# Optimization experiments

Measured on AMD Instinct MI355X. Metric: run time of the kernel, lower is better.

The kernel has to match this reference:

```python
import jax, jax.numpy as jnp
import numpy as np

HIDDEN = 64
N_HEADS = 4
TOP_K = 10
ALPHA = 0.3


def setup_inputs() -> dict:
    key = jax.random.key(0)
    ks = jax.random.split(key, 12)
    B, N, T, Dd, Ds, H = 4, 2048, 32, 16, 8, HIDDEN
    s = lambda i, shape, scale: (jax.random.normal(ks[i], shape, dtype=jnp.float32) * scale)
    return {
        "x_dyn": jax.random.normal(ks[0], (B, N, T, Dd), dtype=jnp.float32),
        "x_stat": jax.random.normal(ks[1], (B, N, Ds), dtype=jnp.float32),
        "A_prior": jax.random.uniform(ks[2], (B, N, N), dtype=jnp.float32),
        "W_dyn": s(3, (Dd, H), 1.0 / np.sqrt(Dd)),
        "b_dyn": jnp.zeros((H,), jnp.float32),
        "W_stat": s(4, (Ds, H), 1.0 / np.sqrt(Ds)),
        "b_stat": jnp.zeros((H,), jnp.float32),
        "W_fuse": s(5, (2 * H, H), 1.0 / np.sqrt(2 * H)),
        "b_fuse": jnp.zeros((H,), jnp.float32),
        "Wq": s(6, (H, H), 1.0 / np.sqrt(H)),
        "Wk": s(7, (H, H), 1.0 / np.sqrt(H)),
    }


def reference(x_dyn, x_stat, A_prior, W_dyn, b_dyn, W_stat, b_stat, W_fuse, b_fuse, Wq, Wk):
    B, N = x_dyn.shape[0], x_dyn.shape[1]
    H, nh = HIDDEN, N_HEADS
    dh = H // nh

    # TemporalEncoder: linear + mean over time + ReLU -> (B, N, H)
    h = jax.nn.relu(jnp.mean(x_dyn @ W_dyn + b_dyn, axis=2))
    # FeatureEncoder: linear + ReLU -> (B, N, H)
    h_s = jax.nn.relu(x_stat @ W_stat + b_stat)
    # Fusion
    h = jnp.concatenate([h, h_s], axis=-1) @ W_fuse + b_fuse

    # GraphAttention: multi-head softmax(QK^T / sqrt(dh)) averaged over heads
    q = (h @ Wq).reshape(B, N, nh, dh)
    k = (h @ Wk).reshape(B, N, nh, dh)
    scores = jnp.einsum("bnhd,bmhd->bhnm", q, k) / jnp.sqrt(jnp.float32(dh))
    A_learn = jnp.mean(jax.nn.softmax(scores, axis=-1), axis=1)  # (B, N, N)

    # Top-k mask along last dim (scatter 1s at topk indices)
    _, topk_inds = jax.lax.top_k(A_learn, TOP_K)  # (B, N, k)
    b_idx = jnp.arange(B)[:, None, None]
    n_idx = jnp.arange(N)[None, :, None]
    mask = jnp.zeros_like(A_learn).at[b_idx, n_idx, topk_inds].set(1.0)
    A_sparse = A_learn * mask
    A_learn = (A_sparse + jnp.swapaxes(A_sparse, 1, 2)) * 0.5

    # Blend with prior
    A_final = ALPHA * A_prior + (1.0 - ALPHA) * A_learn

    # Laplacian L = D - A
    degree = jnp.sum(A_final, axis=-1)  # (B, N)
    eye = jnp.eye(N, dtype=A_final.dtype)
    L = degree[..., None] * eye - A_final
    return (L, A_final)
```

## Files before the change

kernel.cpp:

```cpp
#include <hip/hip_runtime.h>

#define NBATCH 4
#define NN 2048
#define NR 8192
#define TOPK 10
#define CSTRIDE 321

typedef __attribute__((ext_vector_type(16))) float f32x16;
typedef __attribute__((ext_vector_type(8))) short bf16x8;

__device__ inline unsigned short f2bf(float x) {
    unsigned u = __float_as_uint(x);
    unsigned r = (u + 0x7FFF + ((u >> 16) & 1)) >> 16;
    return (unsigned short)r;
}

__global__ __launch_bounds__(256) void k13(
    const float* __restrict__ xd, const float* __restrict__ xs,
    const float* __restrict__ Wd, const float* __restrict__ bd,
    const float* __restrict__ Ws, const float* __restrict__ bs,
    const float* __restrict__ Wf, const float* __restrict__ bf,
    const float* __restrict__ Wq, const float* __restrict__ Wk,
    unsigned short* __restrict__ qh, unsigned short* __restrict__ kh,
    const float* __restrict__ prior, float* __restrict__ Lout,
    float* __restrict__ Aout)
{
    if (blockIdx.x >= NR/4) {
        int r = blockIdx.x - NR/4;
        __shared__ float wsum[4];
        const float4* pr = (const float4*)(prior + (size_t)r * NN);
        float4* Ar = (float4*)(Aout + (size_t)r * NN);
        float4* Lr = (float4*)(Lout + (size_t)r * NN);
        float sum = 0.f;
        for (int i = threadIdx.x; i < NN/4; i += 256) {
            float4 p = pr[i];
            float4 a; a.x = 0.3f*p.x; a.y = 0.3f*p.y; a.z = 0.3f*p.z; a.w = 0.3f*p.w;
            Ar[i] = a;
            float4 lv; lv.x = -a.x; lv.y = -a.y; lv.z = -a.z; lv.w = -a.w;
            Lr[i] = lv;
            sum += a.x + a.y + a.z + a.w;
        }
        #pragma unroll
        for (int o = 32; o > 0; o >>= 1) sum += __shfl_down(sum, o);
        if ((threadIdx.x & 63) == 0) wsum[threadIdx.x >> 6] = sum;
        __syncthreads();
        if (threadIdx.x == 0) {
            float tot = wsum[0] + wsum[1] + wsum[2] + wsum[3];
            atomicAdd(&Lout[(size_t)r * NN + (r & 2047)], tot);
        }
        return;
    }

    int wave = threadIdx.x >> 6;
    int lane = threadIdx.x & 63;
    int r = blockIdx.x * 4 + wave;

    __shared__ float xm[4][16];
    __shared__ float xst[4][8];
    __shared__ float hc[4][128];
    __shared__ float hh[4][64];

    const float* xdr = xd + (size_t)r * 512;
    float acc = 0.f;
    #pragma unroll
    for (int j = 0; j < 8; ++j) acc += xdr[lane + 64*j];
    acc += __shfl_xor(acc, 16);
    acc += __shfl_xor(acc, 32);
    if (lane < 16) xm[wave][lane] = acc * (1.0f/32.0f);
    if (lane < 8)  xst[wave][lane] = xs[(size_t)r*8 + lane];
    __syncthreads();

    float a1 = bd[lane];
    #pragma unroll
    for (int d = 0; d < 16; ++d) a1 += xm[wave][d] * Wd[d*64 + lane];
    a1 = fmaxf(a1, 0.f);
    float a2 = bs[lane];
    #pragma unroll
    for (int d = 0; d < 8; ++d) a2 += xst[wave][d] * Ws[d*64 + lane];
    a2 = fmaxf(a2, 0.f);
    hc[wave][lane] = a1;
    hc[wave][64 + lane] = a2;
    __syncthreads();

    float hv0 = bf[lane], hv1 = 0.f, hv2 = 0.f, hv3 = 0.f;
    #pragma unroll
    for (int j = 0; j < 128; j += 4) {
        hv0 += hc[wave][j]   * Wf[(j)*64   + lane];
        hv1 += hc[wave][j+1] * Wf[(j+1)*64 + lane];
        hv2 += hc[wave][j+2] * Wf[(j+2)*64 + lane];
        hv3 += hc[wave][j+3] * Wf[(j+3)*64 + lane];
    }
    hh[wave][lane] = (hv0 + hv1) + (hv2 + hv3);
    __syncthreads();

    float qv0 = 0.f, qv1 = 0.f, kv0 = 0.f, kv1 = 0.f;
    #pragma unroll
    for (int j = 0; j < 64; j += 2) {
        float h0 = hh[wave][j], h1 = hh[wave][j+1];
        qv0 += h0 * Wq[(j)*64   + lane];
        qv1 += h1 * Wq[(j+1)*64 + lane];
        kv0 += h0 * Wk[(j)*64   + lane];
        kv1 += h1 * Wk[(j+1)*64 + lane];
    }
    float qv = qv0 + qv1, kv = kv0 + kv1;
    int b = r >> 11, n = r & 2047;
    int head = lane >> 4, dim = lane & 15;
    size_t base = ((size_t)(b*4 + head) * NN + n) * 16;
    qh[base + dim] = f2bf(qv);
    kh[base + dim] = f2bf(kv);
}

__global__ __launch_bounds__(1024, 4) void k2_fused(
    const unsigned short* __restrict__ qh, const unsigned short* __restrict__ kh,
    float* __restrict__ Lout, float* __restrict__ Aout)
{
    const float C1 = 0.36067376022224085f;
    int b  = blockIdx.x >> 6;
    int rg = blockIdx.x & 63;
    int tid = threadIdx.x;
    int w = tid >> 6, l = tid & 63;
    int row = l & 31, khalf = l >> 5;

    __shared__ unsigned cand[32 * CSTRIDE];
    __shared__ float redS[16][4][32];
    __shared__ float r4s[4][32];

    bf16x8 qfrag[4];
    #pragma unroll
    for (int h = 0; h < 4; ++h)
        qfrag[h] = *(const bf16x8*)(qh + ((size_t)(b*4+h) * NN + rg*32 + row) * 16 + khalf*8);

    float Sl[4] = {0.f, 0.f, 0.f, 0.f};
    for (int t = 0; t < 4; ++t) {
        int m0 = w*128 + t*32;
        #pragma unroll
        for (int h = 0; h < 4; ++h) {
            bf16x8 kfrag = *(const bf16x8*)(kh + ((size_t)(b*4+h) * NN + m0 + row) * 16 + khalf*8);
            f32x16 acc = {0.f,0.f,0.f,0.f,0.f,0.f,0.f,0.f,0.f,0.f,0.f,0.f,0.f,0.f,0.f,0.f};
            acc = __builtin_amdgcn_mfma_f32_32x32x16_bf16(kfrag, qfrag[h], acc, 0, 0, 0);
            #pragma unroll
            for (int rr = 0; rr < 16; ++rr) Sl[h] += exp2f(acc[rr] * C1);
        }
    }
    #pragma unroll
    for (int h = 0; h < 4; ++h) Sl[h] += __shfl_xor(Sl[h], 32);
    if (l < 32) {
        #pragma unroll
        for (int h = 0; h < 4; ++h) redS[w][h][l] = Sl[h];
    }
    __syncthreads();
    if (tid < 128) {
        int h = tid >> 5, rw = tid & 31;
        float s = 0.f;
        #pragma unroll
        for (int ww = 0; ww < 16; ++ww) s += redS[ww][h][rw];
        r4s[h][rw] = 0.25f / s;
    }
    __syncthreads();

    float r4[4];
    #pragma unroll
    for (int h = 0; h < 4; ++h) r4[h] = r4s[h][row];

    unsigned tkl[TOPK];
    #pragma unroll
    for (int s = 0; s < TOPK; ++s) tkl[s] = 0u;
    for (int t = 0; t < 4; ++t) {
        int m0 = w*128 + t*32;
        float vacc[16];
        #pragma unroll
        for (int rr = 0; rr < 16; ++rr) vacc[rr] = 0.f;
        #pragma unroll
        for (int h = 0; h < 4; ++h) {
            bf16x8 kfrag = *(const bf16x8*)(kh + ((size_t)(b*4+h) * NN + m0 + row) * 16 + khalf*8);
            f32x16 acc = {0.f,0.f,0.f,0.f,0.f,0.f,0.f,0.f,0.f,0.f,0.f,0.f,0.f,0.f,0.f,0.f};
            acc = __builtin_amdgcn_mfma_f32_32x32x16_bf16(kfrag, qfrag[h], acc, 0, 0, 0);
            #pragma unroll
            for (int rr = 0; rr < 16; ++rr)
                vacc[rr] = fmaf(exp2f(acc[rr] * C1), r4[h], vacc[rr]);
        }
        #pragma unroll
        for (int rr = 0; rr < 16; ++rr) {
            int c = m0 + ((rr & 3) + 8*(rr >> 2) + 4*khalf);
            unsigned key = ((unsigned)f2bf(vacc[rr]) << 16) | (unsigned)(2047 - c);
            if (key > tkl[TOPK-1]) {
                unsigned ck = key;
                #pragma unroll
                for (int s = 0; s < TOPK; ++s) {
                    bool ins = ck > tkl[s];
                    unsigned o = tkl[s];
                    tkl[s] = ins ? ck : o;
                    ck     = ins ? o  : ck;
                }
            }
        }
    }
    {
        unsigned* cr = &cand[row * CSTRIDE + (w*2 + khalf) * TOPK];
        #pragma unroll
        for (int s = 0; s < TOPK; ++s) cr[s] = tkl[s];
    }
    __syncthreads();

    #pragma unroll 1
    for (int rr2 = 0; rr2 < 2; ++rr2) {
        int prow = w*2 + rr2;
        const unsigned* flat = &cand[prow * CSTRIDE];
        unsigned tk5[5];
        #pragma unroll
        for (int i = 0; i < 5; ++i) tk5[i] = flat[l*5 + i];
        unsigned mykey = 0u;
        #pragma unroll 1
        for (int s = 0; s < TOPK; ++s) {
            unsigned kmax = tk5[0];
            #pragma unroll
            for (int d = 1; d < 64; d <<= 1) {
                unsigned o = __shfl_xor(kmax, d);
                kmax = (o > kmax) ? o : kmax;
            }
            if (tk5[0] == kmax) {
                #pragma unroll
                for (int q = 0; q < 4; ++q) tk5[q] = tk5[q+1];
                tk5[4] = 0u;
            }
            if (l == s) mykey = kmax;
        }

        int n = rg*32 + prow;
        size_t rbase = (size_t)(b*NN + n) * NN;
        float wv = 0.f;
        int j = 0;
        if (l < TOPK) {
            wv = 0.35f * __uint_as_float(mykey & 0xFFFF0000u);
            j = 2047 - (int)(mykey & 0x7FFu);
        }
        float swv = wv;
        #pragma unroll
        for (int d = 1; d <= 8; d <<= 1) swv += __shfl_xor(swv, d);
        if (l == 0) atomicAdd(&Lout[rbase + n], swv);
        if (l < TOPK) {
            size_t jbase = (size_t)(b*NN + j) * NN;
            atomicAdd(&Aout[rbase + j],  wv);
            atomicAdd(&Aout[jbase + n],  wv);
            atomicAdd(&Lout[rbase + j], -wv);
            atomicAdd(&Lout[jbase + n], -wv);
            atomicAdd(&Lout[jbase + j],  wv);
        }
    }
}

extern "C" void kernel_launch(void* const* d_in, const int* in_sizes, int n_in,
                              void* d_out, int out_size, void* d_ws, size_t ws_size,
                              hipStream_t stream)
{
    const float* xd    = (const float*)d_in[0];
    const float* xs    = (const float*)d_in[1];
    const float* prior = (const float*)d_in[2];
    const float* Wd    = (const float*)d_in[3];
    const float* bd    = (const float*)d_in[4];
    const float* Ws    = (const float*)d_in[5];
    const float* bs    = (const float*)d_in[6];
    const float* Wf    = (const float*)d_in[7];
    const float* bf    = (const float*)d_in[8];
    const float* Wq    = (const float*)d_in[9];
    const float* Wk    = (const float*)d_in[10];

    float* Lout = (float*)d_out;
    float* Aout = Lout + (size_t)NR * NN;

    unsigned short* qh = (unsigned short*)d_ws;
    unsigned short* kh = qh + (size_t)16 * NN * 16;

    k13<<<NR/4 + NR, 256, 0, stream>>>(xd, xs, Wd, bd, Ws, bs, Wf, bf, Wq, Wk,
                                       qh, kh, prior, Lout, Aout);
    k2_fused<<<NBATCH*64, 1024, 0, stream>>>(qh, kh, Lout, Aout);
}
```

Baseline: 324.0 us.

## Overlap prior blend with attention kernel and defer top-k scatter to separate kernel

Moves the prior-blend/Laplacian-init blocks from the encoder kernel into the attention/top-k kernel so the bandwidth-bound streaming overlaps with the MFMA-heavy score computation. The attention blocks shrink from 1024 to 512 threads, each wave covering twice the columns. Top-k winners are written to a workspace buffer and scattered by a new third kernel, which also avoids racing the atomics against the prior initialisation. This adds one launch and a small workspace round trip, and gives fewer waves per attention block.

```diff
diff --git a/kernel.cpp b/kernel.cpp
--- a/kernel.cpp
+++ b/kernel.cpp
@@ -4,7 +4,7 @@
 #define NN 2048
 #define NR 8192
 #define TOPK 10
-#define CSTRIDE 321
+#define CSTRIDE 161
 
 typedef __attribute__((ext_vector_type(16))) float f32x16;
 typedef __attribute__((ext_vector_type(8))) short bf16x8;
@@ -15,42 +15,14 @@
     return (unsigned short)r;
 }
 
-__global__ __launch_bounds__(256) void k13(
+__global__ __launch_bounds__(256) void k1_encode(
     const float* __restrict__ xd, const float* __restrict__ xs,
     const float* __restrict__ Wd, const float* __restrict__ bd,
     const float* __restrict__ Ws, const float* __restrict__ bs,
     const float* __restrict__ Wf, const float* __restrict__ bf,
     const float* __restrict__ Wq, const float* __restrict__ Wk,
-    unsigned short* __restrict__ qh, unsigned short* __restrict__ kh,
-    const float* __restrict__ prior, float* __restrict__ Lout,
-    float* __restrict__ Aout)
-{
-    if (blockIdx.x >= NR/4) {
-        int r = blockIdx.x - NR/4;
-        __shared__ float wsum[4];
-        const float4* pr = (const float4*)(prior + (size_t)r * NN);
-        float4* Ar = (float4*)(Aout + (size_t)r * NN);
-        float4* Lr = (float4*)(Lout + (size_t)r * NN);
-        float sum = 0.f;
-        for (int i = threadIdx.x; i < NN/4; i += 256) {
-            float4 p = pr[i];
-            float4 a; a.x = 0.3f*p.x; a.y = 0.3f*p.y; a.z = 0.3f*p.z; a.w = 0.3f*p.w;
-            Ar[i] = a;
-            float4 lv; lv.x = -a.x; lv.y = -a.y; lv.z = -a.z; lv.w = -a.w;
-            Lr[i] = lv;
-            sum += a.x + a.y + a.z + a.w;
-        }
-        #pragma unroll
-        for (int o = 32; o > 0; o >>= 1) sum += __shfl_down(sum, o);
-        if ((threadIdx.x & 63) == 0) wsum[threadIdx.x >> 6] = sum;
-        __syncthreads();
-        if (threadIdx.x == 0) {
-            float tot = wsum[0] + wsum[1] + wsum[2] + wsum[3];
-            atomicAdd(&Lout[(size_t)r * NN + (r & 2047)], tot);
-        }
-        return;
-    }
-
+    unsigned short* __restrict__ qh, unsigned short* __restrict__ kh)
+{
     int wave = threadIdx.x >> 6;
     int lane = threadIdx.x & 63;
     int r = blockIdx.x * 4 + wave;
@@ -110,19 +82,47 @@
     kh[base + dim] = f2bf(kv);
 }
 
-__global__ __launch_bounds__(1024, 4) void k2_fused(
+__global__ __launch_bounds__(512, 4) void k23(
     const unsigned short* __restrict__ qh, const unsigned short* __restrict__ kh,
-    float* __restrict__ Lout, float* __restrict__ Aout)
+    unsigned* __restrict__ winners, float* __restrict__ diagw,
+    const float* __restrict__ prior, float* __restrict__ Lout,
+    float* __restrict__ Aout)
 {
     const float C1 = 0.36067376022224085f;
+    int tid = threadIdx.x;
+
+    if (blockIdx.x >= 256) {
+        int r = blockIdx.x - 256;
+        __shared__ float wsum[8];
+        const float4* pr = (const float4*)(prior + (size_t)r * NN);
+        float4* Ar = (float4*)(Aout + (size_t)r * NN);
+        float4* Lr = (float4*)(Lout + (size_t)r * NN);
+        float4 p = pr[tid];
+        float4 a; a.x = 0.3f*p.x; a.y = 0.3f*p.y; a.z = 0.3f*p.z; a.w = 0.3f*p.w;
+        Ar[tid] = a;
+        float4 lv; lv.x = -a.x; lv.y = -a.y; lv.z = -a.z; lv.w = -a.w;
+        Lr[tid] = lv;
+        float sum = a.x + a.y + a.z + a.w;
+        #pragma unroll
+        for (int o = 32; o > 0; o >>= 1) sum += __shfl_down(sum, o);
+        if ((tid & 63) == 0) wsum[tid >> 6] = sum;
+        __syncthreads();
+        if (tid == 0) {
+            float tot = 0.f;
+            #pragma unroll
+            for (int ww = 0; ww < 8; ++ww) tot += wsum[ww];
+            atomicAdd(&Lout[(size_t)r * NN + (r & 2047)], tot);
+        }
+        return;
+    }
+
     int b  = blockIdx.x >> 6;
     int rg = blockIdx.x & 63;
-    int tid = threadIdx.x;
     int w = tid >> 6, l = tid & 63;
     int row = l & 31, khalf = l >> 5;
 
     __shared__ unsigned cand[32 * CSTRIDE];
-    __shared__ float redS[16][4][32];
+    __shared__ float redS[8][4][32];
     __shared__ float r4s[4][32];
 
     bf16x8 qfrag[4];
@@ -131,8 +131,8 @@
         qfrag[h] = *(const bf16x8*)(qh + ((size_t)(b*4+h) * NN + rg*32 + row) * 16 + khalf*8);
 
     float Sl[4] = {0.f, 0.f, 0.f, 0.f};
-    for (int t = 0; t < 4; ++t) {
-        int m0 = w*128 + t*32;
+    for (int t = 0; t < 8; ++t) {
+        int m0 = w*256 + t*32;
         #pragma unroll
         for (int h = 0; h < 4; ++h) {
             bf16x8 kfrag = *(const bf16x8*)(kh + ((size_t)(b*4+h) * NN + m0 + row) * 16 + khalf*8);
@@ -153,7 +153,7 @@
         int h = tid >> 5, rw = tid & 31;
         float s = 0.f;
         #pragma unroll
-        for (int ww = 0; ww < 16; ++ww) s += redS[ww][h][rw];
+        for (int ww = 0; ww < 8; ++ww) s += redS[ww][h][rw];
         r4s[h][rw] = 0.25f / s;
     }
     __syncthreads();
@@ -165,8 +165,8 @@
     unsigned tkl[TOPK];
     #pragma unroll
     for (int s = 0; s < TOPK; ++s) tkl[s] = 0u;
-    for (int t = 0; t < 4; ++t) {
-        int m0 = w*128 + t*32;
+    for (int t = 0; t < 8; ++t) {
+        int m0 = w*256 + t*32;
         float vacc[16];
         #pragma unroll
         for (int rr = 0; rr < 16; ++rr) vacc[rr] = 0.f;
@@ -203,50 +203,59 @@
     __syncthreads();
 
     #pragma unroll 1
-    for (int rr2 = 0; rr2 < 2; ++rr2) {
-        int prow = w*2 + rr2;
+    for (int rr2 = 0; rr2 < 4; ++rr2) {
+        int prow = w*4 + rr2;
         const unsigned* flat = &cand[prow * CSTRIDE];
-        unsigned tk5[5];
-        #pragma unroll
-        for (int i = 0; i < 5; ++i) tk5[i] = flat[l*5 + i];
+        unsigned t0 = flat[l];
+        unsigned t1 = flat[l + 64];
+        unsigned t2 = (l < 32) ? flat[l + 128] : 0u;
+        if (t1 > t0) { unsigned x = t0; t0 = t1; t1 = x; }
+        if (t2 > t1) { unsigned x = t1; t1 = t2; t2 = x; }
+        if (t1 > t0) { unsigned x = t0; t0 = t1; t1 = x; }
         unsigned mykey = 0u;
         #pragma unroll 1
         for (int s = 0; s < TOPK; ++s) {
-            unsigned kmax = tk5[0];
+            unsigned kmax = t0;
             #pragma unroll
             for (int d = 1; d < 64; d <<= 1) {
                 unsigned o = __shfl_xor(kmax, d);
                 kmax = (o > kmax) ? o : kmax;
             }
-            if (tk5[0] == kmax) {
-                #pragma unroll
-                for (int q = 0; q < 4; ++q) tk5[q] = tk5[q+1];
-                tk5[4] = 0u;
-            }
+            if (t0 == kmax) { t0 = t1; t1 = t2; t2 = 0u; }
             if (l == s) mykey = kmax;
         }
 
         int n = rg*32 + prow;
-        size_t rbase = (size_t)(b*NN + n) * NN;
-        float wv = 0.f;
-        int j = 0;
-        if (l < TOPK) {
-            wv = 0.35f * __uint_as_float(mykey & 0xFFFF0000u);
-            j = 2047 - (int)(mykey & 0x7FFu);
-        }
+        int r = b*NN + n;
+        float wv = (l < TOPK) ? 0.35f * __uint_as_float(mykey & 0xFFFF0000u) : 0.f;
         float swv = wv;
         #pragma unroll
         for (int d = 1; d <= 8; d <<= 1) swv += __shfl_xor(swv, d);
-        if (l == 0) atomicAdd(&Lout[rbase + n], swv);
-        if (l < TOPK) {
-            size_t jbase = (size_t)(b*NN + j) * NN;
-            atomicAdd(&Aout[rbase + j],  wv);
-            atomicAdd(&Aout[jbase + n],  wv);
-            atomicAdd(&Lout[rbase + j], -wv);
-            atomicAdd(&Lout[jbase + n], -wv);
-            atomicAdd(&Lout[jbase + j],  wv);
-        }
-    }
+        if (l == 0) diagw[r] = swv;
+        if (l < TOPK) winners[(size_t)l * NR + r] = mykey;
+    }
+}
+
+__global__ __launch_bounds__(256) void k4_scatter(
+    const unsigned* __restrict__ winners, const float* __restrict__ diagw,
+    float* __restrict__ Lout, float* __restrict__ Aout)
+{
+    int wk = blockIdx.x * 256 + threadIdx.x;
+    int s = wk >> 13;
+    int r = wk & 8191;
+    int b = r >> 11;
+    int n = r & 2047;
+    unsigned key = winners[(size_t)s * NR + r];
+    float wv = 0.35f * __uint_as_float(key & 0xFFFF0000u);
+    int j = 2047 - (int)(key & 0x7FFu);
+    size_t rbase = (size_t)r * NN;
+    size_t jbase = (size_t)(b * NN + j) * NN;
+    atomicAdd(&Aout[rbase + j],  wv);
+    atomicAdd(&Aout[jbase + n],  wv);
+    atomicAdd(&Lout[rbase + j], -wv);
+    atomicAdd(&Lout[jbase + n], -wv);
+    atomicAdd(&Lout[jbase + j],  wv);
+    if (s == 0) atomicAdd(&Lout[rbase + n], diagw[r]);
 }
 
 extern "C" void kernel_launch(void* const* d_in, const int* in_sizes, int n_in,
@@ -270,8 +279,10 @@
 
     unsigned short* qh = (unsigned short*)d_ws;
     unsigned short* kh = qh + (size_t)16 * NN * 16;
-
-    k13<<<NR/4 + NR, 256, 0, stream>>>(xd, xs, Wd, bd, Ws, bs, Wf, bf, Wq, Wk,
-                                       qh, kh, prior, Lout, Aout);
-    k2_fused<<<NBATCH*64, 1024, 0, stream>>>(qh, kh, Lout, Aout);
-}
+    unsigned* winners  = (unsigned*)(kh + (size_t)16 * NN * 16);
+    float* diagw       = (float*)(winners + (size_t)TOPK * NR);
+
+    k1_encode<<<NR/4, 256, 0, stream>>>(xd, xs, Wd, bd, Ws, bs, Wf, bf, Wq, Wk, qh, kh);
+    k23<<<256 + NR, 512, 0, stream>>>(qh, kh, winners, diagw, prior, Lout, Aout);
+    k4_scatter<<<TOPK*NR/256, 256, 0, stream>>>(winners, diagw, Lout, Aout);
+}
```

Measured after the change: 303.6 us (median of 2 runs). 1.07x faster.
